# Performance work log

Hardware: AMD Instinct MI355X
Metric: run time of the kernel (lower is better)

Reference implementation:

```python
import jax, jax.numpy as jnp
import numpy as np

EPS = 1e-8
NEG = -float(2 ** 31)

B, N, D = 8, 2048, 256  # batch, nodes, input_dim == output_dim


def setup_inputs() -> dict:
    key = jax.random.key(0)
    ks = jax.random.split(key, 8)
    x = jax.random.normal(ks[0], (B, N, D), dtype=jnp.float32)
    x_topic = jax.random.normal(ks[1], (B, N, D), dtype=jnp.float32)
    adj_mask = jax.random.randint(ks[2], (B, N, N), 0, 2, dtype=jnp.int32)
    s = 1.0 / np.sqrt(D)
    W = jax.random.uniform(ks[3], (D, D), minval=-s, maxval=s, dtype=jnp.float32)
    # GRUCell params (torch layout: [3*H, in] with gate order r, z, n)
    W_ih = jax.random.uniform(ks[4], (3 * D, D), minval=-s, maxval=s, dtype=jnp.float32)
    W_hh = jax.random.uniform(ks[5], (3 * D, D), minval=-s, maxval=s, dtype=jnp.float32)
    b_ih = jax.random.uniform(ks[6], (3 * D,), minval=-s, maxval=s, dtype=jnp.float32)
    b_hh = jax.random.uniform(ks[7], (3 * D,), minval=-s, maxval=s, dtype=jnp.float32)
    return {"adj_mask": adj_mask, "x": x, "x_topic": x_topic,
            "W": W, "W_ih": W_ih, "W_hh": W_hh, "b_ih": b_ih, "b_hh": b_hh}


def _gru_cell(inp, h, W_ih, W_hh, b_ih, b_hh):
    # torch.nn.GRUCell math, gate order (r, z, n)
    gi = inp @ W_ih.T + b_ih
    gh = h @ W_hh.T + b_hh
    i_r, i_z, i_n = jnp.split(gi, 3, axis=-1)
    h_r, h_z, h_n = jnp.split(gh, 3, axis=-1)
    r = jax.nn.sigmoid(i_r + h_r)
    z = jax.nn.sigmoid(i_z + h_z)
    n = jnp.tanh(i_n + r * h_n)
    return (1.0 - z) * n + z * h


def reference(adj_mask, x, x_topic, W, W_ih, W_hh, b_ih, b_hh):
    # Wh: [B, N, H]
    Wh = jnp.einsum('bnd,dh->bnh', x, W)
    # pairwise cosine similarity via normalized gram matrix (no N x N x D intermediate)
    nrm = jnp.linalg.norm(x_topic, axis=-1)            # [B, N]
    dots = jnp.einsum('bnd,bmd->bnm', x_topic, x_topic)
    e = dots / jnp.maximum(nrm[:, :, None] * nrm[:, None, :], EPS)
    scores = jnp.where(adj_mask > 0, e, NEG)
    attention = jax.nn.softmax(scores, axis=-1)        # [B, N, N]
    graph_out = jnp.einsum('bnm,bmh->bnh', attention, Wh)
    out = _gru_cell(graph_out, x, W_ih, W_hh, b_ih, b_hh)
    return out
```

## Files before the change

kernel.cpp:

```cpp
#include <hip/hip_runtime.h>
#include <hip/hip_bf16.h>

#define B_ 8
#define N_ 2048
#define D_ 256

using bf16 = __hip_bfloat16;
typedef short v8s __attribute__((ext_vector_type(8)));
typedef float v4f __attribute__((ext_vector_type(4)));
typedef unsigned int u32;
typedef unsigned long long u64;

__device__ __forceinline__ v4f mfma16(v8s a, v8s b, v4f c) {
  return __builtin_amdgcn_mfma_f32_16x16x32_bf16(a, b, c, 0, 0, 0);
}
__device__ __forceinline__ v8s ldb8(const bf16* p) {
  return *reinterpret_cast<const v8s*>(p);
}
__device__ __forceinline__ void glds16(const void* g, void* l) {
  __builtin_amdgcn_global_load_lds((const __attribute__((address_space(1))) u32*)g,
                                   (__attribute__((address_space(3))) u32*)l, 16, 0, 0);
}
__device__ __forceinline__ unsigned short f2bu(float f) {
  bf16 b = __float2bfloat16(f);
  return *reinterpret_cast<unsigned short*>(&b);
}
__device__ __forceinline__ float lo16(u32 u) { union {u32 i; float f;} v; v.i = u << 16; return v.f; }
__device__ __forceinline__ float hi16(u32 u) { union {u32 i; float f;} v; v.i = u & 0xffff0000u; return v.f; }
__device__ __forceinline__ u32 pack2(float a, float b) {
  return (u32)f2bu(a) | ((u32)f2bu(b) << 16);
}
__device__ __forceinline__ float fsigmoid(float x) { return 1.0f / (1.0f + __expf(-x)); }
__device__ __forceinline__ float ftanh(float x) {
  float ax = fabsf(x);
  float t = __expf(-2.0f * ax);
  float r = (1.0f - t) / (1.0f + t);
  return copysignf(r, x);
}

__global__ __launch_bounds__(256) void k_cvt(const float* __restrict__ src,
                                             bf16* __restrict__ dst, int n4) {
  int i = blockIdx.x * 256 + threadIdx.x;
  if (i >= n4) return;
  float4 v = reinterpret_cast<const float4*>(src)[i];
  ushort4 o;
  o.x = f2bu(v.x); o.y = f2bu(v.y); o.z = f2bu(v.z); o.w = f2bu(v.w);
  reinterpret_cast<ushort4*>(dst)[i] = o;
}

__global__ __launch_bounds__(256) void k_cvtn(const float* __restrict__ xt,
                                              bf16* __restrict__ dst,
                                              float* __restrict__ rnorm) {
  int i = blockIdx.x * 256 + threadIdx.x;
  int lane = threadIdx.x & 63;
  float4 v = reinterpret_cast<const float4*>(xt)[i];
  ushort4 o;
  o.x = f2bu(v.x); o.y = f2bu(v.y); o.z = f2bu(v.z); o.w = f2bu(v.w);
  reinterpret_cast<ushort4*>(dst)[i] = o;
  float s = v.x * v.x + v.y * v.y + v.z * v.z + v.w * v.w;
#pragma unroll
  for (int off = 32; off > 0; off >>= 1) s += __shfl_xor(s, off);
  if (lane == 0) rnorm[i >> 6] = 1.0f / fmaxf(sqrtf(s), 1e-8f);
}

__global__ __launch_bounds__(256) void k_pack(const int* __restrict__ adj,
                                              u64* __restrict__ adjp) {
  int wid = (blockIdx.x * 256 + threadIdx.x) >> 6;
  int lane = threadIdx.x & 63;
  const int G = B_ * N_ * (N_ / 64);
#pragma unroll 4
  for (int g = wid; g < G; g += 16384) {
    int v = adj[(size_t)g * 64 + lane];
    u64 m = __ballot(v > 0);
    if (lane == 0) adjp[g] = m;
  }
}

__global__ __launch_bounds__(256) void k_twt(const float* __restrict__ W,
                                             bf16* __restrict__ Wt) {
  int idx = blockIdx.x * 256 + threadIdx.x;
  int d = idx >> 8, h = idx & 255;
  Wt[h * 256 + d] = __float2bfloat16(W[idx]);
}

__global__ __launch_bounds__(256) void k_wht(const bf16* __restrict__ x,
                                             const bf16* __restrict__ Wt,
                                             bf16* __restrict__ WhT) {
  int wid = blockIdx.x * 4 + (threadIdx.x >> 6);
  int lane = threadIdx.x & 63, lr = lane & 15, quad = lane >> 4;
  int b = wid >> 9;
  int rem = wid & 511;
  int h0 = (rem >> 5) << 4;
  int m0 = (rem & 31) << 6;

  v8s a[8];
  const bf16* arow = Wt + (size_t)(h0 + lr) * D_ + quad * 8;
#pragma unroll
  for (int ks = 0; ks < 8; ks++) a[ks] = ldb8(arow + ks * 32);

  const bf16* xb = x + (size_t)b * N_ * D_;
#pragma unroll
  for (int mt = 0; mt < 4; mt++) {
    v4f acc = {0.f, 0.f, 0.f, 0.f};
    const bf16* brow = xb + (size_t)(m0 + mt * 16 + lr) * D_ + quad * 8;
#pragma unroll
    for (int ks = 0; ks < 8; ks++) acc = mfma16(a[ks], ldb8(brow + ks * 32), acc);
    bf16* o = WhT + ((size_t)b * D_ + h0 + quad * 4) * N_ + m0 + mt * 16 + lr;
#pragma unroll
    for (int r = 0; r < 4; r++) o[(size_t)r * N_] = __float2bfloat16(acc[r]);
  }
}

__global__ __launch_bounds__(256, 2) void k_attn(const bf16* __restrict__ xt,
                                                 const u64* __restrict__ adjp,
                                                 const bf16* __restrict__ WhT,
                                                 const float* __restrict__ rnorm,
                                                 bf16* __restrict__ po,
                                                 float* __restrict__ pls) {
  __shared__ __align__(16) bf16 xts[2][32][256];
  __shared__ __align__(16) bf16 whs[2][256][32];
  __shared__ __align__(16) bf16 pbuf[4][16][32];
  __shared__ float rns[1024];

  const int tid = threadIdx.x;
  const int w = tid >> 6, lane = tid & 63, lr = lane & 15, quad = lane >> 4;
  const int b = blockIdx.x & 7;
  const int nt = (blockIdx.x >> 3) & 31;
  const int mh = blockIdx.x >> 8;
  const int n0w = nt * 64 + w * 16;
  const int mbase = mh * 1024;

  const bf16* xtb = xt + (size_t)b * N_ * D_;
  const bf16* whb = WhT + (size_t)b * D_ * N_;
  const float* rnb = rnorm + b * N_;
  const u64* adjb = adjp + (size_t)b * N_ * 32;

  ((float4*)rns)[tid] = ((const float4*)(rnb + mbase))[tid];

  v8s q[8];
  {
    const bf16* qrow = xtb + (size_t)(n0w + lr) * D_ + quad * 8;
#pragma unroll
    for (int kt = 0; kt < 8; kt++) q[kt] = ldb8(qrow + kt * 32);
  }
  float rn[4];
#pragma unroll
  for (int r = 0; r < 4; r++) rn[r] = rnb[n0w + quad * 4 + r];

  auto stage = [&](int d, int m0) {
    const char* gx = (const char*)(xtb + (size_t)m0 * D_);
    char* lx = (char*)(&xts[d][0][0]) + w * 4096;
#pragma unroll
    for (int j = 0; j < 4; j++) {
      int m = w * 8 + j * 2 + (lane >> 5);
      int gg = (lane & 31) ^ (m & 7);
      glds16(gx + (size_t)m * 512 + gg * 16, lx + j * 1024);
    }
    char* lw = (char*)(&whs[d][0][0]) + w * 4096;
#pragma unroll
    for (int j = 0; j < 4; j++) {
      int h = w * 64 + j * 16 + (lane >> 2);
      const char* gw = (const char*)(whb + (size_t)h * N_ + m0) + (lane & 3) * 16;
      glds16(gw, lw + j * 1024);
    }
  };

  u64 mk[4];
  auto ldadj = [&](int ii) {
    int c = mh * 16 + (ii >> 1);
#pragma unroll
    for (int r = 0; r < 4; r++) mk[r] = adjb[(size_t)(n0w + quad * 4 + r) * 32 + c];
  };

  v4f o[16];
#pragma unroll
  for (int t = 0; t < 16; t++) o[t] = (v4f){0, 0, 0, 0};
  float lsum[4] = {0, 0, 0, 0};

  stage(0, mbase);
  ldadj(0);

#pragma unroll 1
  for (int ii = 0; ii < 32; ii++) {
    const int d = ii & 1;
    const int m0 = mbase + ii * 32;
    __syncthreads();
    if (ii + 1 < 32) stage(1 - d, m0 + 32);

    v4f s0 = {0, 0, 0, 0}, s1 = {0, 0, 0, 0};
#pragma unroll
    for (int kt = 0; kt < 8; kt++) {
      int g = ((kt * 4 + quad) ^ (lr & 7)) * 8;
      v8s b0 = ldb8(&xts[d][lr][g]);
      v8s b1 = ldb8(&xts[d][lr + 16][g]);
      s0 = mfma16(q[kt], b0, s0);
      s1 = mfma16(q[kt], b1, s1);
    }

    float rm0 = rns[ii * 32 + lr];
    float rm1 = rns[ii * 32 + 16 + lr];
    const int wsh = (ii & 1) * 32;
    u32 mw[4];
#pragma unroll
    for (int r = 0; r < 4; r++) mw[r] = (u32)(mk[r] >> wsh);
    if (ii + 1 < 32) ldadj(ii + 1);

#pragma unroll
    for (int r = 0; r < 4; r++) {
      float p0 = ((mw[r] >> lr) & 1u)        ? __expf(s0[r] * rn[r] * rm0) : 0.f;
      float p1 = ((mw[r] >> (lr + 16)) & 1u) ? __expf(s1[r] * rn[r] * rm1) : 0.f;
      lsum[r] += p0 + p1;
      pbuf[w][quad * 4 + r][lr]      = __float2bfloat16(p0);
      pbuf[w][quad * 4 + r][lr + 16] = __float2bfloat16(p1);
    }
    v8s pa = ldb8(&pbuf[w][lr][quad * 8]);
#pragma unroll
    for (int ht = 0; ht < 16; ht++) {
      v8s wf = ldb8(&whs[d][ht * 16 + lr][quad * 8]);
      o[ht] = mfma16(pa, wf, o[ht]);
    }
  }

#pragma unroll
  for (int r = 0; r < 4; r++) {
    float t = lsum[r];
    t += __shfl_xor(t, 1); t += __shfl_xor(t, 2);
    t += __shfl_xor(t, 4); t += __shfl_xor(t, 8);
    lsum[r] = t;
  }
  float* plsb = pls + (size_t)mh * (B_ * N_) + (size_t)b * N_;
  if (lr == 0) {
#pragma unroll
    for (int r = 0; r < 4; r++) plsb[n0w + quad * 4 + r] = lsum[r];
  }
  bf16* pob = po + (size_t)mh * ((size_t)B_ * N_ * D_) +
              ((size_t)b * N_ + n0w + quad * 4) * D_ + lr;
#pragma unroll
  for (int r = 0; r < 4; r++) {
#pragma unroll
    for (int ht = 0; ht < 16; ht++) {
      pob[(size_t)r * D_ + ht * 16] = __float2bfloat16(o[ht][r]);
    }
  }
}

__global__ __launch_bounds__(256) void k_comb(const bf16* __restrict__ po,
                                              const float* __restrict__ pls,
                                              bf16* __restrict__ gout) {
  int idx = blockIdx.x * 256 + threadIdx.x;
  int row = idx >> 5;
  float inv = 1.0f / (pls[row] + pls[B_ * N_ + row]);
  const uint4* p0 = (const uint4*)po;
  const uint4* p1 = (const uint4*)(po + (size_t)B_ * N_ * D_);
  uint4 a = p0[idx], c = p1[idx];
  uint4 o;
  o.x = pack2((lo16(a.x) + lo16(c.x)) * inv, (hi16(a.x) + hi16(c.x)) * inv);
  o.y = pack2((lo16(a.y) + lo16(c.y)) * inv, (hi16(a.y) + hi16(c.y)) * inv);
  o.z = pack2((lo16(a.z) + lo16(c.z)) * inv, (hi16(a.z) + hi16(c.z)) * inv);
  o.w = pack2((lo16(a.w) + lo16(c.w)) * inv, (hi16(a.w) + hi16(c.w)) * inv);
  reinterpret_cast<uint4*>(gout)[idx] = o;
}

__global__ __launch_bounds__(256) void k_gru(const bf16* __restrict__ gout,
                                             const bf16* __restrict__ x16,
                                             const bf16* __restrict__ Wih,
                                             const bf16* __restrict__ Whh,
                                             const float* __restrict__ bih,
                                             const float* __restrict__ bhh,
                                             const float* __restrict__ x32,
                                             float* __restrict__ out) {
  int wid = blockIdx.x * 4 + (threadIdx.x >> 6);
  int lane = threadIdx.x & 63, lr = lane & 15, quad = lane >> 4;
  int rs = wid >> 4;
  int col0 = (wid & 15) << 4;
  int row0 = rs << 6;
  int col = col0 + lr;

  float bi[3], bh[3];
#pragma unroll
  for (int g = 0; g < 3; g++) {
    bi[g] = bih[g * 256 + col];
    bh[g] = bhh[g * 256 + col];
  }
  v4f aI[3][4], aH[3][4];
#pragma unroll
  for (int g = 0; g < 3; g++)
#pragma unroll
    for (int rt = 0; rt < 4; rt++) {
      aI[g][rt] = (v4f){0, 0, 0, 0};
      aH[g][rt] = (v4f){0, 0, 0, 0};
    }

#pragma unroll 2
  for (int ks = 0; ks < 8; ks++) {
    int k0 = ks * 32 + quad * 8;
    v8s wI[3], wH[3];
#pragma unroll
    for (int g = 0; g < 3; g++) {
      wI[g] = ldb8(Wih + (size_t)(g * 256 + col0 + lr) * 256 + k0);
      wH[g] = ldb8(Whh + (size_t)(g * 256 + col0 + lr) * 256 + k0);
    }
#pragma unroll
    for (int rt = 0; rt < 4; rt++) {
      v8s aG = ldb8(gout + (size_t)(row0 + rt * 16 + lr) * 256 + k0);
      v8s aX = ldb8(x16 + (size_t)(row0 + rt * 16 + lr) * 256 + k0);
#pragma unroll
      for (int g = 0; g < 3; g++) {
        aI[g][rt] = mfma16(aG, wI[g], aI[g][rt]);
        aH[g][rt] = mfma16(aX, wH[g], aH[g][rt]);
      }
    }
  }

#pragma unroll
  for (int rt = 0; rt < 4; rt++) {
    int rowb = row0 + rt * 16 + quad * 4;
#pragma unroll
    for (int r = 0; r < 4; r++) {
      float ir  = aI[0][rt][r] + bi[0];
      float iz  = aI[1][rt][r] + bi[1];
      float in_ = aI[2][rt][r] + bi[2];
      float hr  = aH[0][rt][r] + bh[0];
      float hz  = aH[1][rt][r] + bh[1];
      float hn  = aH[2][rt][r] + bh[2];
      float rg = fsigmoid(ir + hr);
      float zg = fsigmoid(iz + hz);
      float ng = ftanh(in_ + rg * hn);
      float hv = x32[(size_t)(rowb + r) * 256 + col];
      out[(size_t)(rowb + r) * 256 + col] = (1.0f - zg) * ng + zg * hv;
    }
  }
}

extern "C" void kernel_launch(void* const* d_in, const int* in_sizes, int n_in,
                              void* d_out, int out_size, void* d_ws, size_t ws_size,
                              hipStream_t stream) {
  const int*   adj = (const int*)d_in[0];
  const float* x   = (const float*)d_in[1];
  const float* xt  = (const float*)d_in[2];
  const float* W   = (const float*)d_in[3];
  const float* Wih = (const float*)d_in[4];
  const float* Whh = (const float*)d_in[5];
  const float* bih = (const float*)d_in[6];
  const float* bhh = (const float*)d_in[7];
  float* out = (float*)d_out;

  char* ws = (char*)d_ws;
  bf16*  xb16   = (bf16*)(ws);
  bf16*  xtb16  = (bf16*)(ws + (8u << 20));
  bf16*  gob    = (bf16*)(ws + (16u << 20));
  bf16*  WhT    = (bf16*)(ws + (24u << 20));
  bf16*  Wt     = (bf16*)(ws + (32u << 20));
  bf16*  Wih16  = (bf16*)(ws + (32u << 20) + (128u << 10));
  bf16*  Whh16  = (bf16*)(ws + (32u << 20) + (512u << 10));
  float* rnorm  = (float*)(ws + (32u << 20) + (896u << 10));
  u64*   adjp   = (u64*)  (ws + (32u << 20) + (960u << 10));
  bf16*  po     = (bf16*) (ws + (40u << 20));
  float* pls    = (float*)(ws + (56u << 20));

  const int nBND4 = B_ * N_ * D_ / 4;
  k_pack<<<4096, 256, 0, stream>>>(adj, adjp);
  k_cvt<<<nBND4 / 256, 256, 0, stream>>>(x, xb16, nBND4);
  k_cvtn<<<nBND4 / 256, 256, 0, stream>>>(xt, xtb16, rnorm);
  k_cvt<<<192, 256, 0, stream>>>(Wih, Wih16, 49152);
  k_cvt<<<192, 256, 0, stream>>>(Whh, Whh16, 49152);
  k_twt<<<256, 256, 0, stream>>>(W, Wt);
  k_wht<<<1024, 256, 0, stream>>>(xb16, Wt, WhT);
  k_attn<<<512, 256, 0, stream>>>(xtb16, adjp, WhT, rnorm, po, pls);
  k_comb<<<2048, 256, 0, stream>>>(po, pls, gob);
  k_gru<<<1024, 256, 0, stream>>>(gob, xb16, Wih16, Whh16, bih, bhh, x, out);
}
```

Measured before the change: 400.5 us.

## Rework attention kernel to 32x32 MFMA tiles with 4-way key split

Rewrites k_attn to use 32x32x16 bf16 MFMA, so each wave handles 32 query rows. Key range is split four ways (512 keys per block) instead of two, and k_comb now sums four partials. The adjacency mask is read as 32-bit words and spread across lanes with shuffles. A swizzle is added to the WhT LDS tile, and three small weight-conversion launches are merged into one k_prep kernel. This aims for better MFMA efficiency and reuse per LDS read and fewer launches, at the cost of more partial-output traffic (4x bf16 partials) and higher register pressure. The softmax row sum is now computed from the bf16-rounded probabilities.

```diff
diff --git a/kernel.cpp b/kernel.cpp
--- a/kernel.cpp
+++ b/kernel.cpp
@@ -8,11 +8,15 @@
 using bf16 = __hip_bfloat16;
 typedef short v8s __attribute__((ext_vector_type(8)));
 typedef float v4f __attribute__((ext_vector_type(4)));
+typedef float v16f __attribute__((ext_vector_type(16)));
 typedef unsigned int u32;
 typedef unsigned long long u64;
 
 __device__ __forceinline__ v4f mfma16(v8s a, v8s b, v4f c) {
   return __builtin_amdgcn_mfma_f32_16x16x32_bf16(a, b, c, 0, 0, 0);
+}
+__device__ __forceinline__ v16f mfma32(v8s a, v8s b, v16f c) {
+  return __builtin_amdgcn_mfma_f32_32x32x16_bf16(a, b, c, 0, 0, 0);
 }
 __device__ __forceinline__ v8s ldb8(const bf16* p) {
   return *reinterpret_cast<const v8s*>(p);
@@ -24,6 +28,9 @@
 __device__ __forceinline__ unsigned short f2bu(float f) {
   bf16 b = __float2bfloat16(f);
   return *reinterpret_cast<unsigned short*>(&b);
+}
+__device__ __forceinline__ float bs2f(short s) {
+  union { u32 i; float f; } v; v.i = ((u32)(unsigned short)s) << 16; return v.f;
 }
 __device__ __forceinline__ float lo16(u32 u) { union {u32 i; float f;} v; v.i = u << 16; return v.f; }
 __device__ __forceinline__ float hi16(u32 u) { union {u32 i; float f;} v; v.i = u & 0xffff0000u; return v.f; }
@@ -63,6 +70,32 @@
   if (lane == 0) rnorm[i >> 6] = 1.0f / fmaxf(sqrtf(s), 1e-8f);
 }
 
+__global__ __launch_bounds__(256) void k_prep(const float* __restrict__ W,
+                                              bf16* __restrict__ Wt,
+                                              const float* __restrict__ Wih,
+                                              bf16* __restrict__ Wih16,
+                                              const float* __restrict__ Whh,
+                                              bf16* __restrict__ Whh16) {
+  int blk = blockIdx.x;
+  if (blk < 256) {
+    int idx = blk * 256 + threadIdx.x;
+    int d = idx >> 8, h = idx & 255;
+    Wt[h * 256 + d] = __float2bfloat16(W[idx]);
+  } else if (blk < 448) {
+    int i = (blk - 256) * 256 + threadIdx.x;
+    float4 v = reinterpret_cast<const float4*>(Wih)[i];
+    ushort4 o;
+    o.x = f2bu(v.x); o.y = f2bu(v.y); o.z = f2bu(v.z); o.w = f2bu(v.w);
+    reinterpret_cast<ushort4*>(Wih16)[i] = o;
+  } else {
+    int i = (blk - 448) * 256 + threadIdx.x;
+    float4 v = reinterpret_cast<const float4*>(Whh)[i];
+    ushort4 o;
+    o.x = f2bu(v.x); o.y = f2bu(v.y); o.z = f2bu(v.z); o.w = f2bu(v.w);
+    reinterpret_cast<ushort4*>(Whh16)[i] = o;
+  }
+}
+
 __global__ __launch_bounds__(256) void k_pack(const int* __restrict__ adj,
                                               u64* __restrict__ adjp) {
   int wid = (blockIdx.x * 256 + threadIdx.x) >> 6;
@@ -76,13 +109,6 @@
   }
 }
 
-__global__ __launch_bounds__(256) void k_twt(const float* __restrict__ W,
-                                             bf16* __restrict__ Wt) {
-  int idx = blockIdx.x * 256 + threadIdx.x;
-  int d = idx >> 8, h = idx & 255;
-  Wt[h * 256 + d] = __float2bfloat16(W[idx]);
-}
-
 __global__ __launch_bounds__(256) void k_wht(const bf16* __restrict__ x,
                                              const bf16* __restrict__ Wt,
                                              bf16* __restrict__ WhT) {
@@ -112,134 +138,119 @@
 }
 
 __global__ __launch_bounds__(256, 2) void k_attn(const bf16* __restrict__ xt,
-                                                 const u64* __restrict__ adjp,
+                                                 const u32* __restrict__ adj32,
                                                  const bf16* __restrict__ WhT,
                                                  const float* __restrict__ rnorm,
                                                  bf16* __restrict__ po,
                                                  float* __restrict__ pls) {
-  __shared__ __align__(16) bf16 xts[2][32][256];
-  __shared__ __align__(16) bf16 whs[2][256][32];
-  __shared__ __align__(16) bf16 pbuf[4][16][32];
-  __shared__ float rns[1024];
+  __shared__ __align__(16) bf16 xts[2][32 * 256];
+  __shared__ __align__(16) bf16 whs[2][256 * 32];
+  __shared__ __align__(16) bf16 pbuf[4][32 * 40];
+  __shared__ float rns[512];
 
   const int tid = threadIdx.x;
-  const int w = tid >> 6, lane = tid & 63, lr = lane & 15, quad = lane >> 4;
+  const int w = tid >> 6, lane = tid & 63;
+  const int l5 = lane >> 5, l31 = lane & 31;
   const int b = blockIdx.x & 7;
-  const int nt = (blockIdx.x >> 3) & 31;
-  const int mh = blockIdx.x >> 8;
-  const int n0w = nt * 64 + w * 16;
-  const int mbase = mh * 1024;
+  const int nt = (blockIdx.x >> 3) & 15;
+  const int mh = blockIdx.x >> 7;
+  const int n0w = nt * 128 + w * 32;
+  const int mbase = mh * 512;
 
   const bf16* xtb = xt + (size_t)b * N_ * D_;
   const bf16* whb = WhT + (size_t)b * D_ * N_;
-  const float* rnb = rnorm + b * N_;
-  const u64* adjb = adjp + (size_t)b * N_ * 32;
-
-  ((float4*)rns)[tid] = ((const float4*)(rnb + mbase))[tid];
-
-  v8s q[8];
+
+  if (tid < 128)
+    ((float4*)rns)[tid] = ((const float4*)(rnorm + b * N_ + mbase))[tid];
+
+  v8s q[16];
   {
-    const bf16* qrow = xtb + (size_t)(n0w + lr) * D_ + quad * 8;
-#pragma unroll
-    for (int kt = 0; kt < 8; kt++) q[kt] = ldb8(qrow + kt * 32);
-  }
-  float rn[4];
-#pragma unroll
-  for (int r = 0; r < 4; r++) rn[r] = rnb[n0w + quad * 4 + r];
+    const bf16* qrow = xtb + (size_t)(n0w + l31) * D_ + l5 * 8;
+#pragma unroll
+    for (int kt = 0; kt < 16; kt++) q[kt] = ldb8(qrow + kt * 16);
+  }
+  const float rq = rnorm[b * N_ + n0w + l31];
+  const u32* arow = adj32 + (size_t)(b * N_ + n0w + l31) * 64 + mh * 16;
 
   auto stage = [&](int d, int m0) {
     const char* gx = (const char*)(xtb + (size_t)m0 * D_);
-    char* lx = (char*)(&xts[d][0][0]) + w * 4096;
+    char* lx = ((char*)xts[d]) + w * 4096;
 #pragma unroll
     for (int j = 0; j < 4; j++) {
-      int m = w * 8 + j * 2 + (lane >> 5);
-      int gg = (lane & 31) ^ (m & 7);
+      int m = w * 8 + j * 2 + l5;
+      int gg = l31 ^ (m & 7);
       glds16(gx + (size_t)m * 512 + gg * 16, lx + j * 1024);
     }
-    char* lw = (char*)(&whs[d][0][0]) + w * 4096;
+    char* lw = ((char*)whs[d]) + w * 4096;
 #pragma unroll
     for (int j = 0; j < 4; j++) {
       int h = w * 64 + j * 16 + (lane >> 2);
-      const char* gw = (const char*)(whb + (size_t)h * N_ + m0) + (lane & 3) * 16;
-      glds16(gw, lw + j * 1024);
+      int g = (lane & 3) ^ ((lane >> 2) & 3);
+      glds16((const char*)(whb + (size_t)h * N_ + m0) + g * 16, lw + j * 1024);
     }
   };
 
-  u64 mk[4];
-  auto ldadj = [&](int ii) {
-    int c = mh * 16 + (ii >> 1);
-#pragma unroll
-    for (int r = 0; r < 4; r++) mk[r] = adjb[(size_t)(n0w + quad * 4 + r) * 32 + c];
-  };
-
-  v4f o[16];
-#pragma unroll
-  for (int t = 0; t < 16; t++) o[t] = (v4f){0, 0, 0, 0};
-  float lsum[4] = {0, 0, 0, 0};
-
+  v16f o[8];
+#pragma unroll
+  for (int t = 0; t < 8; t++) o[t] = (v16f)(0.f);
+  float lsum = 0.f;
+
+  u32 mword = arow[0];
   stage(0, mbase);
-  ldadj(0);
 
 #pragma unroll 1
-  for (int ii = 0; ii < 32; ii++) {
+  for (int ii = 0; ii < 16; ii++) {
     const int d = ii & 1;
-    const int m0 = mbase + ii * 32;
     __syncthreads();
-    if (ii + 1 < 32) stage(1 - d, m0 + 32);
-
-    v4f s0 = {0, 0, 0, 0}, s1 = {0, 0, 0, 0};
-#pragma unroll
-    for (int kt = 0; kt < 8; kt++) {
-      int g = ((kt * 4 + quad) ^ (lr & 7)) * 8;
-      v8s b0 = ldb8(&xts[d][lr][g]);
-      v8s b1 = ldb8(&xts[d][lr + 16][g]);
-      s0 = mfma16(q[kt], b0, s0);
-      s1 = mfma16(q[kt], b1, s1);
-    }
-
-    float rm0 = rns[ii * 32 + lr];
-    float rm1 = rns[ii * 32 + 16 + lr];
-    const int wsh = (ii & 1) * 32;
-    u32 mw[4];
-#pragma unroll
-    for (int r = 0; r < 4; r++) mw[r] = (u32)(mk[r] >> wsh);
-    if (ii + 1 < 32) ldadj(ii + 1);
-
-#pragma unroll
-    for (int r = 0; r < 4; r++) {
-      float p0 = ((mw[r] >> lr) & 1u)        ? __expf(s0[r] * rn[r] * rm0) : 0.f;
-      float p1 = ((mw[r] >> (lr + 16)) & 1u) ? __expf(s1[r] * rn[r] * rm1) : 0.f;
-      lsum[r] += p0 + p1;
-      pbuf[w][quad * 4 + r][lr]      = __float2bfloat16(p0);
-      pbuf[w][quad * 4 + r][lr + 16] = __float2bfloat16(p1);
-    }
-    v8s pa = ldb8(&pbuf[w][lr][quad * 8]);
-#pragma unroll
-    for (int ht = 0; ht < 16; ht++) {
-      v8s wf = ldb8(&whs[d][ht * 16 + lr][quad * 8]);
-      o[ht] = mfma16(pa, wf, o[ht]);
-    }
-  }
-
-#pragma unroll
-  for (int r = 0; r < 4; r++) {
-    float t = lsum[r];
-    t += __shfl_xor(t, 1); t += __shfl_xor(t, 2);
-    t += __shfl_xor(t, 4); t += __shfl_xor(t, 8);
-    lsum[r] = t;
-  }
-  float* plsb = pls + (size_t)mh * (B_ * N_) + (size_t)b * N_;
-  if (lr == 0) {
-#pragma unroll
-    for (int r = 0; r < 4; r++) plsb[n0w + quad * 4 + r] = lsum[r];
-  }
-  bf16* pob = po + (size_t)mh * ((size_t)B_ * N_ * D_) +
-              ((size_t)b * N_ + n0w + quad * 4) * D_ + lr;
-#pragma unroll
-  for (int r = 0; r < 4; r++) {
-#pragma unroll
-    for (int ht = 0; ht < 16; ht++) {
-      pob[(size_t)r * D_ + ht * 16] = __float2bfloat16(o[ht][r]);
+    if (ii + 1 < 16) stage(1 - d, mbase + (ii + 1) * 32);
+
+    v16f s = (v16f)(0.f);
+    const bf16* xb = xts[d] + l31 * 256;
+#pragma unroll
+    for (int kt = 0; kt < 16; kt++) {
+      int g = ((kt * 2 + l5) ^ (lane & 7)) * 8;
+      s = mfma32(q[kt], ldb8(xb + g), s);
+    }
+
+    u32 mnext = (ii + 1 < 16) ? arow[ii + 1] : 0u;
+    float rm = rns[ii * 32 + l31];
+
+    bf16* pb = pbuf[w];
+#pragma unroll
+    for (int j = 0; j < 16; j++) {
+      int row = (j & 3) + 8 * (j >> 2) + 4 * l5;
+      u32 mw = __shfl(mword, row);
+      float rnj = __shfl(rq, row);
+      float p = ((mw >> l31) & 1u) ? __expf(s[j] * rnj * rm) : 0.f;
+      pb[row * 40 + l31] = __float2bfloat16(p);
+    }
+    mword = mnext;
+
+    v8s pa0 = ldb8(pb + l31 * 40 + l5 * 8);
+    v8s pa1 = ldb8(pb + l31 * 40 + 16 + l5 * 8);
+#pragma unroll
+    for (int e = 0; e < 8; e++) lsum += bs2f(pa0[e]) + bs2f(pa1[e]);
+
+#pragma unroll
+    for (int ht = 0; ht < 8; ht++) {
+      const bf16* wb = whs[d] + (ht * 32 + l31) * 32;
+      int g0 = (l5 ^ (l31 & 3)) * 8;
+      int g1 = ((2 + l5) ^ (l31 & 3)) * 8;
+      o[ht] = mfma32(pa0, ldb8(wb + g0), o[ht]);
+      o[ht] = mfma32(pa1, ldb8(wb + g1), o[ht]);
+    }
+  }
+
+  lsum += __shfl_xor(lsum, 32);
+  if (lane < 32) pls[(size_t)mh * (B_ * N_) + b * N_ + n0w + l31] = lsum;
+
+  bf16* pob = po + (size_t)mh * ((size_t)B_ * N_ * D_) + ((size_t)b * N_ + n0w) * D_;
+#pragma unroll
+  for (int ht = 0; ht < 8; ht++) {
+#pragma unroll
+    for (int j = 0; j < 16; j++) {
+      int row = (j & 3) + 8 * (j >> 2) + 4 * l5;
+      pob[(size_t)row * D_ + ht * 32 + l31] = __float2bfloat16(o[ht][j]);
     }
   }
 }
@@ -249,15 +260,20 @@
                                               bf16* __restrict__ gout) {
   int idx = blockIdx.x * 256 + threadIdx.x;
   int row = idx >> 5;
-  float inv = 1.0f / (pls[row] + pls[B_ * N_ + row]);
-  const uint4* p0 = (const uint4*)po;
-  const uint4* p1 = (const uint4*)(po + (size_t)B_ * N_ * D_);
-  uint4 a = p0[idx], c = p1[idx];
+  const int R = B_ * N_;
+  float inv = 1.0f / (pls[row] + pls[R + row] + pls[2 * R + row] + pls[3 * R + row]);
+  const size_t S = (size_t)B_ * N_ * D_ / 8;
+  const uint4* p = (const uint4*)po;
+  uint4 a = p[idx], c = p[idx + S], e = p[idx + 2 * S], f = p[idx + 3 * S];
   uint4 o;
-  o.x = pack2((lo16(a.x) + lo16(c.x)) * inv, (hi16(a.x) + hi16(c.x)) * inv);
-  o.y = pack2((lo16(a.y) + lo16(c.y)) * inv, (hi16(a.y) + hi16(c.y)) * inv);
-  o.z = pack2((lo16(a.z) + lo16(c.z)) * inv, (hi16(a.z) + hi16(c.z)) * inv);
-  o.w = pack2((lo16(a.w) + lo16(c.w)) * inv, (hi16(a.w) + hi16(c.w)) * inv);
+  o.x = pack2((lo16(a.x)+lo16(c.x)+lo16(e.x)+lo16(f.x)) * inv,
+              (hi16(a.x)+hi16(c.x)+hi16(e.x)+hi16(f.x)) * inv);
+  o.y = pack2((lo16(a.y)+lo16(c.y)+lo16(e.y)+lo16(f.y)) * inv,
+              (hi16(a.y)+hi16(c.y)+hi16(e.y)+hi16(f.y)) * inv);
+  o.z = pack2((lo16(a.z)+lo16(c.z)+lo16(e.z)+lo16(f.z)) * inv,
+              (hi16(a.z)+hi16(c.z)+hi16(e.z)+hi16(f.z)) * inv);
+  o.w = pack2((lo16(a.w)+lo16(c.w)+lo16(e.w)+lo16(f.w)) * inv,
+              (hi16(a.w)+hi16(c.w)+hi16(e.w)+hi16(f.w)) * inv);
   reinterpret_cast<uint4*>(gout)[idx] = o;
 }
 
@@ -356,17 +372,15 @@
   float* rnorm  = (float*)(ws + (32u << 20) + (896u << 10));
   u64*   adjp   = (u64*)  (ws + (32u << 20) + (960u << 10));
   bf16*  po     = (bf16*) (ws + (40u << 20));
-  float* pls    = (float*)(ws + (56u << 20));
+  float* pls    = (float*)(ws + (72u << 20));
 
   const int nBND4 = B_ * N_ * D_ / 4;
   k_pack<<<4096, 256, 0, stream>>>(adj, adjp);
   k_cvt<<<nBND4 / 256, 256, 0, stream>>>(x, xb16, nBND4);
   k_cvtn<<<nBND4 / 256, 256, 0, stream>>>(xt, xtb16, rnorm);
-  k_cvt<<<192, 256, 0, stream>>>(Wih, Wih16, 49152);
-  k_cvt<<<192, 256, 0, stream>>>(Whh, Whh16, 49152);
-  k_twt<<<256, 256, 0, stream>>>(W, Wt);
+  k_prep<<<640, 256, 0, stream>>>(W, Wt, Wih, Wih16, Whh, Whh16);
   k_wht<<<1024, 256, 0, stream>>>(xb16, Wt, WhT);
-  k_attn<<<512, 256, 0, stream>>>(xtb16, adjp, WhT, rnorm, po, pls);
+  k_attn<<<512, 256, 0, stream>>>(xtb16, (const u32*)adjp, WhT, rnorm, po, pls);
   k_comb<<<2048, 256, 0, stream>>>(po, pls, gob);
   k_gru<<<1024, 256, 0, stream>>>(gob, xb16, Wih16, Whh16, bih, bhh, x, out);
 }
```

Measured after the change: 423.0 us. 5.6% more time.
